# Kernel optimization log

Measured on AMD Instinct MI355X. Metric: run time of the kernel, lower is better.

Reference implementation:

```python
import jax, jax.numpy as jnp
import numpy as np

B, T, H, C = 32, 2048, 200, 256

def conv1d(x, w):
    # x: [B, T, Cin], w: [K, Cin, Cout], padding SAME, stride 1
    return jax.lax.conv_general_dilated(x, w, (1,), 'SAME',
                                        dimension_numbers=('NWC', 'WIO', 'NWC'))

def reverse_sequence(x, lengths):
    # tf.reverse_sequence along time axis 1
    t = jnp.arange(x.shape[1])[None, :]          # [1, T]
    L = lengths[:, None]                          # [B, 1]
    idx = jnp.where(t < L, L - 1 - t, t)          # [B, T]
    return jnp.take_along_axis(x, idx[:, :, None], axis=1)

def lstm(x, lengths, W, b):
    # BasicLSTMCell: gates [i, j, f, o], forget_bias=1.0
    xT = jnp.transpose(x, (1, 0, 2))              # [T, B, C]
    c0 = jnp.zeros((x.shape[0], H), x.dtype)
    h0 = jnp.zeros((x.shape[0], H), x.dtype)
    def step(carry, inp):
        c, h = carry
        xt, t = inp
        z = jnp.concatenate([xt, h], -1) @ W + b  # [B, 4H]
        i, j, f, o = jnp.split(z, 4, axis=-1)
        c_new = c * jax.nn.sigmoid(f + 1.0) + jax.nn.sigmoid(i) * jnp.tanh(j)
        h_new = jnp.tanh(c_new) * jax.nn.sigmoid(o)
        m = (t < lengths)[:, None]
        c2 = jnp.where(m, c_new, c)
        h2 = jnp.where(m, h_new, h)
        out = jnp.where(m, h_new, jnp.zeros_like(h_new))
        return (c2, h2), out
    _, ys = jax.lax.scan(step, (c0, h0), (xT, jnp.arange(xT.shape[0])))
    return jnp.transpose(ys, (1, 0, 2))           # [B, T, H]

def setup_inputs() -> dict:
    key = jax.random.key(0)
    ks = jax.random.split(key, 12)
    s = lambda k, shape, fan_in: jax.random.normal(k, shape, jnp.float32) * (1.0 / np.sqrt(fan_in))
    return {
        'signals': jax.random.normal(ks[0], (B, T, 1), jnp.float32),
        'sig_length': jax.random.randint(ks[1], (B,), T // 2, T + 1),
        'k1w': s(ks[2], (1, 1, C), 1),
        'k1aw': s(ks[3], (1, 1, C), 1),
        'k1ab': jnp.zeros((C,), jnp.float32),
        'k2w': s(ks[4], (3, C, C), 3 * C),
        'k3w': s(ks[5], (1, C, C), C),
        'Wf': s(ks[6], (C + H, 4 * H), C + H),
        'bf': jnp.zeros((4 * H,), jnp.float32),
        'Wb': s(ks[7], (C + H, 4 * H), C + H),
        'bb': jnp.zeros((4 * H,), jnp.float32),
        'Wd': s(ks[8], (2 * H, 5), 2 * H),
        'bd': jnp.zeros((5,), jnp.float32),
    }

def reference(signals, sig_length, k1w, k1aw, k1ab, k2w, k3w, Wf, bf, Wb, bb, Wd, bd):
    # resBlock
    conv1 = jax.nn.relu(conv1d(signals, k1w))
    conv1a = jax.nn.relu(conv1d(signals, k1aw) + k1ab)
    conv2 = jax.nn.relu(conv1d(conv1, k2w))
    conv3 = jax.nn.relu(conv1d(conv2, k3w))
    enc = conv3 + conv1a                               # [B, T, 256]
    # bidirectional LSTM
    fw = lstm(enc, sig_length, Wf, bf)                 # [B, T, 200]
    x_rev = reverse_sequence(enc, sig_length)
    bw = reverse_sequence(lstm(x_rev, sig_length, Wb, bb), sig_length)
    bi = jnp.concatenate([fw, bw], -1)                 # [B, T, 400]
    # dense decode to 5 logits (4 bases + blank)
    logits = bi @ Wd + bd                              # [B, T, 5]
    return logits
```

## Files before the change

### kernel.cpp

```cpp
#include <hip/hip_runtime.h>
#include <cstdint>

#define T_LEN 2048
#define NB    32
#define NROWS (NB*T_LEN)
#define HH    200
#define G4    800
#define TB    128
#define SB    8
#define XWSZ  ((size_t)64 * TB * 800)

typedef _Float16 f16;
typedef _Float16 f16x2 __attribute__((ext_vector_type(2)));
typedef _Float16 f16x8 __attribute__((ext_vector_type(8)));
typedef float   floatx4 __attribute__((ext_vector_type(4)));

#define GLD_LDS16(g, l) __builtin_amdgcn_global_load_lds( \
    (const __attribute__((address_space(1))) void*)(g), \
    (__attribute__((address_space(3))) void*)(l), 16, 0, 0)

static __device__ __forceinline__ unsigned short f2h(float x) {
  f16 h = (f16)x; return __builtin_bit_cast(unsigned short, h);
}
static __device__ __forceinline__ float dot2f(unsigned int a, unsigned int b, float c) {
  return __builtin_amdgcn_fdot2(__builtin_bit_cast(f16x2, a),
                                __builtin_bit_cast(f16x2, b), c, false);
}
static __device__ __forceinline__ float sigm(float x) {
  return __builtin_amdgcn_rcpf(1.f + __expf(-x));
}
static __device__ __forceinline__ float tanh_fast(float x) {
  return 1.f - 2.f * __builtin_amdgcn_rcpf(__expf(2.f * x) + 1.f);
}

__global__ void pq_kernel(const float* __restrict__ k1w, const float* __restrict__ k2w,
                          float* __restrict__ PQ) {
  int id = blockIdx.x * 256 + threadIdx.x;
  int pq = id / 768;
  int rem = id % 768;
  int wdt = rem / 256;
  int co  = rem % 256;
  float acc = 0.f;
  for (int ci = 0; ci < 256; ++ci) {
    float k = k1w[ci];
    float kk = pq ? fmaxf(-k, 0.f) : fmaxf(k, 0.f);
    acc += kk * k2w[((size_t)wdt * 256 + ci) * 256 + co];
  }
  PQ[id] = acc;
}

__global__ void prep_kernel(const float* __restrict__ k3w,
                            const float* __restrict__ Wf, const float* __restrict__ bfv,
                            const float* __restrict__ Wb, const float* __restrict__ bbv,
                            unsigned short* __restrict__ K3h, unsigned short* __restrict__ Wx2,
                            unsigned short* __restrict__ WhK, float* __restrict__ bcat) {
  int id = blockIdx.x * 256 + threadIdx.x;
  if (id < 65536) {
    K3h[id] = f2h(k3w[(id & 255) * 256 + (id >> 8)]);
    return;
  }
  id -= 65536;
  if (id < 409600) {
    int dirv = id / 204800;
    int r = id % 204800;
    int c = r >> 8, k = r & 255;
    int n = c >> 2, q = c & 3;
    int g = q * 200 + n;
    const float* W = dirv ? Wb : Wf;
    Wx2[id] = f2h(W[k * 800 + g]);
    return;
  }
  id -= 409600;
  if (id < 320000) {
    int rec = id / 160;
    int m   = id % 160;
    int g   = m / 40, j = m % 40;
    int n   = rec % 200;
    int t2  = rec / 200;
    int s   = t2 % 5, dirv = t2 / 5;
    int k   = s * 40 + j;
    const float* W = dirv ? Wb : Wf;
    WhK[id] = f2h(W[(256 + k) * 800 + (g * 200 + n)]);
    return;
  }
  id -= 320000;
  if (id < 1600) {
    int dirv = id / 800;
    int c = id % 800;
    int n = c >> 2, q = c & 3;
    int g = q * 200 + n;
    bcat[id] = (dirv ? bbv : bfv)[g] + (q == 2 ? 1.f : 0.f);
  }
}

__global__ void conv2_kernel(const float* __restrict__ s, const float* __restrict__ PQ,
                             unsigned short* __restrict__ C2) {
  int row = blockIdx.x;
  int co  = threadIdx.x;
  int t = row & (T_LEN - 1);
  float s0 = s[row];
  float sm = (t > 0)         ? s[row - 1] : 0.f;
  float sp = (t < T_LEN - 1) ? s[row + 1] : 0.f;
  const float* P = PQ;
  const float* Q = PQ + 768;
  float acc = 0.f;
  float a, m;
  a = fmaxf(sm, 0.f); m = fmaxf(-sm, 0.f);
  acc += a * P[0*256+co] + m * Q[0*256+co];
  a = fmaxf(s0, 0.f); m = fmaxf(-s0, 0.f);
  acc += a * P[1*256+co] + m * Q[1*256+co];
  a = fmaxf(sp, 0.f); m = fmaxf(-sp, 0.f);
  acc += a * P[2*256+co] + m * Q[2*256+co];
  C2[(size_t)row * 256 + co] = f2h(fmaxf(acc, 0.f));
}

__global__ __launch_bounds__(256, 2) void gemm_kernel(
    const unsigned short* __restrict__ Ag, const unsigned short* __restrict__ Bg0,
    int N, int ntiles, int mode,
    unsigned short* __restrict__ Outp,
    const float* __restrict__ bias, const float* __restrict__ Sg,
    const float* __restrict__ k1aw, const float* __restrict__ k1ab,
    const int* __restrict__ lens, int t0)
{
  __shared__ __align__(16) unsigned short Bl[128*128];
  __shared__ __align__(16) unsigned short Al[128*40];
  __shared__ int rowsrc[128];
  int tid = threadIdx.x;
  int tm = blockIdx.x / ntiles, tn = blockIdx.x % ntiles;
  int col0 = tn * 128;
  int lane = tid & 63, wv = tid >> 6;
  int quad = lane >> 4, l16 = lane & 15;
  int wrow = (wv & 1) * 64, wcol = (wv >> 1) * 64;

  int dirv = 0;
  if (mode == 2) dirv = tm >> 5;
  const unsigned short* Bg = Bg0 + (size_t)dirv * 204800;

  if (tid < 128) {
    int r;
    if (mode == 2) {
      int m = tm * 128 + tid;
      int ch = m >> 7;
      int ls = m & 127;
      int b = ch & 31, dd = ch >> 5;
      int L = lens[b]; L = (L < 0) ? 0 : ((L > T_LEN) ? T_LEN : L);
      int t = t0 + ls;
      int src = dd ? (L - 1 - t) : t;
      src = (src < 0) ? 0 : ((src > T_LEN - 1) ? (T_LEN - 1) : src);
      r = b * T_LEN + src;
    } else {
      r = tm * 128 + tid;
    }
    rowsrc[tid] = r;
  }

  floatx4 acc[16];
  #pragma unroll
  for (int i = 0; i < 16; ++i) acc[i] = (floatx4){0.f,0.f,0.f,0.f};

  for (int ph = 0; ph < 2; ++ph) {
    __syncthreads();
    #pragma unroll
    for (int it = 0; it < 8; ++it) {
      int idx = it * 256 + tid;
      int n  = idx >> 4;
      int k8 = idx & 15;
      int nn = col0 + n;
      uint4 v = (uint4){0u,0u,0u,0u};
      if (nn < N) v = *(const uint4*)(Bg + (size_t)nn * 256 + ph * 128 + k8 * 8);
      *(uint4*)(&Bl[n * 128 + ((k8 ^ (n & 7)) * 8)]) = v;
    }
    for (int kb2 = 0; kb2 < 4; ++kb2) {
      int kb = ph * 4 + kb2;
      __syncthreads();
      #pragma unroll
      for (int i = 0; i < 2; ++i) {
        int c2 = i * 256 + tid;
        int r = c2 >> 2, kc = (c2 & 3) * 8;
        uint4 v = *(const uint4*)(Ag + (size_t)rowsrc[r] * 256 + kb * 32 + kc);
        *(uint4*)(&Al[r * 40 + kc]) = v;
      }
      __syncthreads();
      f16x8 af[4], bfr[4];
      #pragma unroll
      for (int mt = 0; mt < 4; ++mt)
        af[mt] = *(const f16x8*)(&Al[(wrow + mt*16 + l16) * 40 + quad * 8]);
      #pragma unroll
      for (int nt = 0; nt < 4; ++nt) {
        int nl = wcol + nt*16 + l16;
        int c = kb2 * 4 + quad;
        bfr[nt] = *(const f16x8*)(&Bl[nl * 128 + ((c ^ (nl & 7)) * 8)]);
      }
      #pragma unroll
      for (int mt = 0; mt < 4; ++mt)
        #pragma unroll
        for (int nt = 0; nt < 4; ++nt)
          acc[mt*4+nt] = __builtin_amdgcn_mfma_f32_16x16x32_f16(af[mt], bfr[nt], acc[mt*4+nt], 0, 0, 0);
    }
  }
  #pragma unroll
  for (int mt = 0; mt < 4; ++mt) {
    #pragma unroll
    for (int nt = 0; nt < 4; ++nt) {
      floatx4 v = acc[mt*4+nt];
      int col = col0 + wcol + nt*16 + l16;
      if (col < N) {
        #pragma unroll
        for (int r = 0; r < 4; ++r) {
          int row = tm * 128 + wrow + mt*16 + quad*4 + r;
          float x = v[r];
          float o;
          if (mode == 0) {
            float sv = Sg[row];
            float a1 = sv * k1aw[col] + k1ab[col];
            o = fmaxf(x, 0.f) + fmaxf(a1, 0.f);
          } else {
            o = x + bias[dirv * 800 + col];
          }
          Outp[(size_t)row * N + col] = f2h(o);
        }
      }
    }
  }
}

__global__ __launch_bounds__(1024, 4)
void mega_kernel(
    const unsigned short* __restrict__ Eg,
    const unsigned short* __restrict__ Wx2,
    unsigned short* __restrict__ XWbuf,
    const float* __restrict__ bcat,
    const unsigned short* __restrict__ WhK,
    const int* __restrict__ lens,
    unsigned short* __restrict__ fwH, unsigned short* __restrict__ bwH,
    float* __restrict__ cState, unsigned short* __restrict__ hState,
    int k)
{
  __shared__ __align__(16) unsigned short xw_lds[2][SB*800];
  __shared__ __align__(16) unsigned short hist[SB*200];
  __shared__ __align__(16) unsigned short himg[2][200];
  __shared__ __align__(16) floatx4 zp[800];
  __shared__ __align__(16) unsigned short Bl[128*128];
  __shared__ __align__(16) unsigned short Al[128*40];
  __shared__ int rowsrc[128];

  int tid = threadIdx.x;
  int t0 = k * TB;

  if (blockIdx.x < 64) {
    int ch  = blockIdx.x;
    int dir = ch >> 5;
    int b   = ch & 31;
    int L = lens[b];
    L = (L < 0) ? 0 : ((L > T_LEN) ? T_LEN : L);
    int tend = t0 + TB; if (tend > L) tend = L;
    bool worker = tid < 1000;
    int s = tid / 200;
    int n = tid - s * 200;

    if (tid < 200) ((unsigned int*)himg)[tid] = 0u;

    float c = 0.f;
    unsigned short last_h = 0;
    if (tid < 200 && t0 > 0) {
      c = cState[ch * HH + tid];
      last_h = hState[ch * HH + tid];
    }
    __syncthreads();
    if (tid < 200 && t0 > 0) himg[0][tid] = last_h;

    unsigned int w[80];
    if (worker) {
      const uint4* wp = (const uint4*)(WhK + ((size_t)((dir * 5 + s) * 200 + n)) * 160);
      #pragma unroll
      for (int r = 0; r < 20; ++r) {
        uint4 v = wp[r];
        w[4*r+0] = v.x; w[4*r+1] = v.y; w[4*r+2] = v.z; w[4*r+3] = v.w;
      }
      #pragma unroll
      for (int r = 0; r < 80; ++r)
        asm volatile("" : "+v"(w[r]));
    }

    unsigned short* Hd = dir ? bwH : fwH;
    const unsigned short* XWc = XWbuf + (size_t)(k & 1) * XWSZ + ((size_t)ch * TB) * 800;

    if (t0 < tend && tid < 800)
      GLD_LDS16(XWc + (size_t)tid * 8, &xw_lds[0][tid * 8]);
    __syncthreads();

    int buf = 0, cur = 0;
    int prev_tb = -1, prev_cnt = 0;

    for (int tb = t0; tb < tend; tb += SB) {
      int cnt = tend - tb; if (cnt > SB) cnt = SB;
      for (int sl = 0; sl < cnt; ++sl) {
        if (sl == 0) {
          int ntb = tb + SB;
          if ((ntb - t0) < TB && tid < 800) {
            const unsigned short* src = XWc + (size_t)(ntb - t0) * 800;
            GLD_LDS16(src + (size_t)tid * 8, &xw_lds[buf ^ 1][tid * 8]);
          }
          if (prev_tb >= 0) {
            int pcnt = prev_cnt;
            if (tid < pcnt * 25) {
              int srow = dir ? (pcnt - 1 - tid / 25) : (tid / 25);
              uint4 v = *(const uint4*)&hist[srow*200 + (tid % 25)*8];
              size_t base = dir ? ((size_t)(b*T_LEN + (L - prev_tb - pcnt)))*HH
                                : ((size_t)(b*T_LEN + prev_tb))*HH;
              *(uint4*)(Hd + base + (size_t)tid*8) = v;
            }
          }
        }
        float a0 = 0.f, a1 = 0.f, a2 = 0.f, a3 = 0.f;
        if (worker) {
          const uint4* hp = (const uint4*)(&himg[cur][s * 40]);
          #pragma unroll
          for (int r = 0; r < 5; ++r) {
            uint4 hv = hp[r];
            int d = r * 4;
            a0 = dot2f(hv.x, w[d],      a0); a1 = dot2f(hv.x, w[20 + d], a1);
            a2 = dot2f(hv.x, w[40 + d], a2); a3 = dot2f(hv.x, w[60 + d], a3);
            a0 = dot2f(hv.y, w[d + 1],  a0); a1 = dot2f(hv.y, w[21 + d], a1);
            a2 = dot2f(hv.y, w[41 + d], a2); a3 = dot2f(hv.y, w[61 + d], a3);
            a0 = dot2f(hv.z, w[d + 2],  a0); a1 = dot2f(hv.z, w[22 + d], a1);
            a2 = dot2f(hv.z, w[42 + d], a2); a3 = dot2f(hv.z, w[62 + d], a3);
            a0 = dot2f(hv.w, w[d + 3],  a0); a1 = dot2f(hv.w, w[23 + d], a1);
            a2 = dot2f(hv.w, w[43 + d], a2); a3 = dot2f(hv.w, w[63 + d], a3);
          }
          if (s != 0) {
            floatx4 z; z[0] = a0; z[1] = a1; z[2] = a2; z[3] = a3;
            zp[(s - 1) * 200 + n] = z;
          }
        }
        __syncthreads();
        if (tid < 200) {
          floatx4 p0 = zp[tid], p1 = zp[200 + tid], p2 = zp[400 + tid], p3 = zp[600 + tid];
          uint2 xv = *(const uint2*)&xw_lds[buf][sl*800 + 4*tid];
          f16x2 xa = __builtin_bit_cast(f16x2, xv.x);
          f16x2 xb = __builtin_bit_cast(f16x2, xv.y);
          float zi = a0 + p0[0] + p1[0] + p2[0] + p3[0] + (float)xa[0];
          float zj = a1 + p0[1] + p1[1] + p2[1] + p3[1] + (float)xa[1];
          float zf = a2 + p0[2] + p1[2] + p2[2] + p3[2] + (float)xb[0];
          float zo = a3 + p0[3] + p1[3] + p2[3] + p3[3] + (float)xb[1];
          c = c * sigm(zf) + sigm(zi) * tanh_fast(zj);
          float h = tanh_fast(c) * sigm(zo);
          unsigned short hh = f2h(h);
          last_h = hh;
          himg[cur ^ 1][tid] = hh;
          hist[sl*200 + tid] = hh;
        }
        cur ^= 1;
        __syncthreads();
      }
      prev_tb = tb; prev_cnt = cnt; buf ^= 1;
    }
    if (prev_tb >= 0) {
      int pcnt = prev_cnt;
      if (tid < pcnt * 25) {
        int srow = dir ? (pcnt - 1 - tid / 25) : (tid / 25);
        uint4 v = *(const uint4*)&hist[srow*200 + (tid % 25)*8];
        size_t base = dir ? ((size_t)(b*T_LEN + (L - prev_tb - pcnt)))*HH
                          : ((size_t)(b*T_LEN + prev_tb))*HH;
        *(uint4*)(Hd + base + (size_t)tid*8) = v;
      }
    }
    if (tid < 200) {
      cState[ch * HH + tid] = c;
      hState[ch * HH + tid] = last_h;
    }
    return;
  }

  int tgem = t0 + TB;
  if (tgem >= T_LEN) return;
  unsigned short* Outp = XWbuf + (size_t)((k + 1) & 1) * XWSZ;
  int lane = tid & 63, wv = tid >> 6;
  int quad = lane >> 4, l16 = lane & 15;
  int wrow = (wv & 1) * 64, wcol = (wv >> 1) * 64;

  for (int task = blockIdx.x - 64; task < 448; task += 150) {
    int tm = task / 7, tn = task % 7;
    int col0 = tn * 128;
    int dirv = tm >> 5;
    const unsigned short* Bg = Wx2 + (size_t)dirv * 204800;

    __syncthreads();
    if (tid < 128) {
      int m = tm * 128 + tid;
      int chn = m >> 7;
      int ls = m & 127;
      int bb = chn & 31, dd = chn >> 5;
      int L = lens[bb]; L = (L < 0) ? 0 : ((L > T_LEN) ? T_LEN : L);
      int t = tgem + ls;
      int src = dd ? (L - 1 - t) : t;
      src = (src < 0) ? 0 : ((src > T_LEN - 1) ? (T_LEN - 1) : src);
      rowsrc[tid] = bb * T_LEN + src;
    }

    floatx4 acc[16];
    #pragma unroll
    for (int i = 0; i < 16; ++i) acc[i] = (floatx4){0.f,0.f,0.f,0.f};

    for (int ph = 0; ph < 2; ++ph) {
      __syncthreads();
      if (tid < 256) {
        #pragma unroll
        for (int it = 0; it < 8; ++it) {
          int idx = it * 256 + tid;
          int nl = idx >> 4;
          int k8 = idx & 15;
          int nn = col0 + nl;
          uint4 v = (uint4){0u,0u,0u,0u};
          if (nn < 800) v = *(const uint4*)(Bg + (size_t)nn * 256 + ph * 128 + k8 * 8);
          *(uint4*)(&Bl[nl * 128 + ((k8 ^ (nl & 7)) * 8)]) = v;
        }
      }
      for (int kb2 = 0; kb2 < 4; ++kb2) {
        int kb = ph * 4 + kb2;
        __syncthreads();
        if (tid < 256) {
          #pragma unroll
          for (int i = 0; i < 2; ++i) {
            int c2 = i * 256 + tid;
            int r = c2 >> 2, kc = (c2 & 3) * 8;
            uint4 v = *(const uint4*)(Eg + (size_t)rowsrc[r] * 256 + kb * 32 + kc);
            *(uint4*)(&Al[r * 40 + kc]) = v;
          }
        }
        __syncthreads();
        if (tid < 256) {
          f16x8 af[4], bfr[4];
          #pragma unroll
          for (int mt = 0; mt < 4; ++mt)
            af[mt] = *(const f16x8*)(&Al[(wrow + mt*16 + l16) * 40 + quad * 8]);
          #pragma unroll
          for (int nt = 0; nt < 4; ++nt) {
            int nl = wcol + nt*16 + l16;
            int cx = kb2 * 4 + quad;
            bfr[nt] = *(const f16x8*)(&Bl[nl * 128 + ((cx ^ (nl & 7)) * 8)]);
          }
          #pragma unroll
          for (int mt = 0; mt < 4; ++mt)
            #pragma unroll
            for (int nt = 0; nt < 4; ++nt)
              acc[mt*4+nt] = __builtin_amdgcn_mfma_f32_16x16x32_f16(af[mt], bfr[nt], acc[mt*4+nt], 0, 0, 0);
        }
      }
    }
    if (tid < 256) {
      #pragma unroll
      for (int mt = 0; mt < 4; ++mt) {
        #pragma unroll
        for (int nt = 0; nt < 4; ++nt) {
          floatx4 v = acc[mt*4+nt];
          int col = col0 + wcol + nt*16 + l16;
          if (col < 800) {
            #pragma unroll
            for (int r = 0; r < 4; ++r) {
              int row = tm * 128 + wrow + mt*16 + quad*4 + r;
              Outp[(size_t)row * 800 + col] = f2h(v[r] + bcat[dirv * 800 + col]);
            }
          }
        }
      }
    }
  }
}

__global__ __launch_bounds__(256) void out_kernel(
    const unsigned short* __restrict__ fwH, const unsigned short* __restrict__ bwH,
    const float* __restrict__ Wd, const float* __restrict__ bd, float* __restrict__ out)
{
  __shared__ float wd[2000];
  int tid = threadIdx.x;
  for (int i = tid; i < 2000; i += 256) wd[i] = Wd[i];
  __syncthreads();
  int row = blockIdx.x * 256 + tid;
  float acc0 = bd[0], acc1 = bd[1], acc2 = bd[2], acc3 = bd[3], acc4 = bd[4];
  const unsigned int* fu = (const unsigned int*)(fwH + (size_t)row * HH);
  const unsigned int* bu = (const unsigned int*)(bwH + (size_t)row * HH);
  #pragma unroll 4
  for (int i = 0; i < 100; ++i) {
    f16x2 pf = __builtin_bit_cast(f16x2, fu[i]);
    f16x2 pb = __builtin_bit_cast(f16x2, bu[i]);
    int k = 2 * i;
    float f0 = (float)pf[0], f1 = (float)pf[1];
    float b0 = (float)pb[0], b1 = (float)pb[1];
    const float* w0 = &wd[k*5];
    const float* w1 = &wd[(k+1)*5];
    const float* w2 = &wd[(200+k)*5];
    const float* w3 = &wd[(201+k)*5];
    acc0 += f0*w0[0] + f1*w1[0] + b0*w2[0] + b1*w3[0];
    acc1 += f0*w0[1] + f1*w1[1] + b0*w2[1] + b1*w3[1];
    acc2 += f0*w0[2] + f1*w1[2] + b0*w2[2] + b1*w3[2];
    acc3 += f0*w0[3] + f1*w1[3] + b0*w2[3] + b1*w3[3];
    acc4 += f0*w0[4] + f1*w1[4] + b0*w2[4] + b1*w3[4];
  }
  float* o = out + (size_t)row * 5;
  o[0]=acc0; o[1]=acc1; o[2]=acc2; o[3]=acc3; o[4]=acc4;
}

extern "C" void kernel_launch(void* const* d_in, const int* in_sizes, int n_in,
                              void* d_out, int out_size, void* d_ws, size_t ws_size,
                              hipStream_t stream)
{
  const float* signals = (const float*)d_in[0];
  const int*   lens    = (const int*)  d_in[1];
  const float* k1w     = (const float*)d_in[2];
  const float* k1aw    = (const float*)d_in[3];
  const float* k1ab    = (const float*)d_in[4];
  const float* k2w     = (const float*)d_in[5];
  const float* k3w     = (const float*)d_in[6];
  const float* Wf      = (const float*)d_in[7];
  const float* bf      = (const float*)d_in[8];
  const float* Wb      = (const float*)d_in[9];
  const float* bb      = (const float*)d_in[10];
  const float* Wd      = (const float*)d_in[11];
  const float* bd      = (const float*)d_in[12];
  float* out = (float*)d_out;
  char* ws = (char*)d_ws;

  size_t szC2   = (size_t)NROWS * 256 * 2;
  size_t szXWb  = 2 * XWSZ * 2;
  size_t szA    = (szC2 > szXWb) ? szC2 : szXWb;
  size_t oA   = 0;
  size_t oE   = oA   + szA;
  size_t oFw  = oE   + (size_t)NROWS*256*2;
  size_t oBw  = oFw  + (size_t)NROWS*HH*2;
  size_t oWhK = oBw  + (size_t)NROWS*HH*2;
  size_t oWx2 = oWhK + (size_t)320000*2;
  size_t oK3  = oWx2 + (size_t)2*256*800*2;
  size_t oPQ  = oK3  + (size_t)256*256*2;
  size_t oBc  = oPQ  + 1536*4;
  size_t oCst = oBc  + 1600*4;
  size_t oHst = oCst + (size_t)64*HH*4;
  size_t total= oHst + (size_t)64*HH*2;
  if (ws_size < total) return;

  unsigned short* C2    = (unsigned short*)(ws + oA);
  unsigned short* XWbuf = (unsigned short*)(ws + oA);
  unsigned short* E     = (unsigned short*)(ws + oE);
  unsigned short* fwH   = (unsigned short*)(ws + oFw);
  unsigned short* bwH   = (unsigned short*)(ws + oBw);
  unsigned short* WhK   = (unsigned short*)(ws + oWhK);
  unsigned short* Wx2   = (unsigned short*)(ws + oWx2);
  unsigned short* K3h   = (unsigned short*)(ws + oK3);
  float* PQ     = (float*)(ws + oPQ);
  float* bcat   = (float*)(ws + oBc);
  float* cState = (float*)(ws + oCst);
  unsigned short* hState = (unsigned short*)(ws + oHst);

  (void)hipMemsetAsync(fwH, 0, (size_t)2*NROWS*HH*2, stream);
  pq_kernel  <<<6,     256, 0, stream>>>(k1w, k2w, PQ);
  prep_kernel<<<3113,  256, 0, stream>>>(k3w, Wf, bf, Wb, bb, K3h, Wx2, WhK, bcat);
  conv2_kernel<<<NROWS, 256, 0, stream>>>(signals, PQ, C2);
  gemm_kernel<<<1024,  256, 0, stream>>>(C2, K3h, 256, 2, 0, E, nullptr, signals, k1aw, k1ab, nullptr, 0);
  gemm_kernel<<<448,   256, 0, stream>>>(E, Wx2, 800, 7, 2, XWbuf, bcat, nullptr, nullptr, nullptr, lens, 0);
  for (int k = 0; k < T_LEN / TB; ++k) {
    mega_kernel<<<214, 1024, 0, stream>>>(E, Wx2, XWbuf, bcat, WhK, lens, fwH, bwH, cState, hState, k);
  }
  out_kernel <<<256,   256, 0, stream>>>(fwH, bwH, Wd, bd, out);
}
```

Baseline: 2.347 ms.

## Process two time chunks per mega_kernel launch using a four-buffer XW ring

Each mega_kernel launch now runs the recurrence across nc consecutive 128-step chunks and has the GEMM blocks precompute input projections for the next nc chunks. XW buffering grows to four slots when the workspace allows it. This halves the number of launches and grid-wide sync points, cutting per-launch overhead and the cost of reloading weights into registers. In exchange it needs more workspace and the GEMM work per launch is larger, which could unbalance the recurrent and GEMM blocks.

```diff
diff --git a/kernel.cpp b/kernel.cpp
--- a/kernel.cpp
+++ b/kernel.cpp
@@ -234,7 +234,7 @@
     const int* __restrict__ lens,
     unsigned short* __restrict__ fwH, unsigned short* __restrict__ bwH,
     float* __restrict__ cState, unsigned short* __restrict__ hState,
-    int k)
+    int k, int nc, int bmask)
 {
   __shared__ __align__(16) unsigned short xw_lds[2][SB*800];
   __shared__ __align__(16) unsigned short hist[SB*200];
@@ -245,7 +245,6 @@
   __shared__ int rowsrc[128];
 
   int tid = threadIdx.x;
-  int t0 = k * TB;
 
   if (blockIdx.x < 64) {
     int ch  = blockIdx.x;
@@ -253,10 +252,10 @@
     int b   = ch & 31;
     int L = lens[b];
     L = (L < 0) ? 0 : ((L > T_LEN) ? T_LEN : L);
-    int tend = t0 + TB; if (tend > L) tend = L;
     bool worker = tid < 1000;
     int s = tid / 200;
     int n = tid - s * 200;
+    int t0 = k * TB;
 
     if (tid < 200) ((unsigned int*)himg)[tid] = 0u;
 
@@ -283,77 +282,82 @@
     }
 
     unsigned short* Hd = dir ? bwH : fwH;
-    const unsigned short* XWc = XWbuf + (size_t)(k & 1) * XWSZ + ((size_t)ch * TB) * 800;
-
-    if (t0 < tend && tid < 800)
-      GLD_LDS16(XWc + (size_t)tid * 8, &xw_lds[0][tid * 8]);
-    __syncthreads();
-
-    int buf = 0, cur = 0;
+    int cur = 0;
     int prev_tb = -1, prev_cnt = 0;
 
-    for (int tb = t0; tb < tend; tb += SB) {
-      int cnt = tend - tb; if (cnt > SB) cnt = SB;
-      for (int sl = 0; sl < cnt; ++sl) {
-        if (sl == 0) {
-          int ntb = tb + SB;
-          if ((ntb - t0) < TB && tid < 800) {
-            const unsigned short* src = XWc + (size_t)(ntb - t0) * 800;
-            GLD_LDS16(src + (size_t)tid * 8, &xw_lds[buf ^ 1][tid * 8]);
-          }
-          if (prev_tb >= 0) {
-            int pcnt = prev_cnt;
-            if (tid < pcnt * 25) {
-              int srow = dir ? (pcnt - 1 - tid / 25) : (tid / 25);
-              uint4 v = *(const uint4*)&hist[srow*200 + (tid % 25)*8];
-              size_t base = dir ? ((size_t)(b*T_LEN + (L - prev_tb - pcnt)))*HH
-                                : ((size_t)(b*T_LEN + prev_tb))*HH;
-              *(uint4*)(Hd + base + (size_t)tid*8) = v;
+    for (int kk = k; kk < k + nc; ++kk) {
+      int t0c = kk * TB;
+      int tend = t0c + TB; if (tend > L) tend = L;
+      const unsigned short* XWc = XWbuf + (size_t)(kk & bmask) * XWSZ + ((size_t)ch * TB) * 800;
+
+      if (t0c < tend && tid < 800)
+        GLD_LDS16(XWc + (size_t)tid * 8, &xw_lds[0][tid * 8]);
+      __syncthreads();
+
+      int buf = 0;
+      for (int tb = t0c; tb < tend; tb += SB) {
+        int cnt = tend - tb; if (cnt > SB) cnt = SB;
+        for (int sl = 0; sl < cnt; ++sl) {
+          if (sl == 0) {
+            int ntb = tb + SB;
+            if ((ntb - t0c) < TB && tid < 800) {
+              const unsigned short* src = XWc + (size_t)(ntb - t0c) * 800;
+              GLD_LDS16(src + (size_t)tid * 8, &xw_lds[buf ^ 1][tid * 8]);
             }
-          }
+            if (prev_tb >= 0) {
+              int pcnt = prev_cnt;
+              if (tid < pcnt * 25) {
+                int srow = dir ? (pcnt - 1 - tid / 25) : (tid / 25);
+                uint4 v = *(const uint4*)&hist[srow*200 + (tid % 25)*8];
+                size_t base = dir ? ((size_t)(b*T_LEN + (L - prev_tb - pcnt)))*HH
+                                  : ((size_t)(b*T_LEN + prev_tb))*HH;
+                *(uint4*)(Hd + base + (size_t)tid*8) = v;
+              }
+            }
+          }
+          float a0 = 0.f, a1 = 0.f, a2 = 0.f, a3 = 0.f;
+          if (worker) {
+            const uint4* hp = (const uint4*)(&himg[cur][s * 40]);
+            #pragma unroll
+            for (int r = 0; r < 5; ++r) {
+              uint4 hv = hp[r];
+              int d = r * 4;
+              a0 = dot2f(hv.x, w[d],      a0); a1 = dot2f(hv.x, w[20 + d], a1);
+              a2 = dot2f(hv.x, w[40 + d], a2); a3 = dot2f(hv.x, w[60 + d], a3);
+              a0 = dot2f(hv.y, w[d + 1],  a0); a1 = dot2f(hv.y, w[21 + d], a1);
+              a2 = dot2f(hv.y, w[41 + d], a2); a3 = dot2f(hv.y, w[61 + d], a3);
+              a0 = dot2f(hv.z, w[d + 2],  a0); a1 = dot2f(hv.z, w[22 + d], a1);
+              a2 = dot2f(hv.z, w[42 + d], a2); a3 = dot2f(hv.z, w[62 + d], a3);
+              a0 = dot2f(hv.w, w[d + 3],  a0); a1 = dot2f(hv.w, w[23 + d], a1);
+              a2 = dot2f(hv.w, w[43 + d], a2); a3 = dot2f(hv.w, w[63 + d], a3);
+            }
+            if (s != 0) {
+              floatx4 z; z[0] = a0; z[1] = a1; z[2] = a2; z[3] = a3;
+              zp[(s - 1) * 200 + n] = z;
+            }
+          }
+          __syncthreads();
+          if (tid < 200) {
+            floatx4 p0 = zp[tid], p1 = zp[200 + tid], p2 = zp[400 + tid], p3 = zp[600 + tid];
+            uint2 xv = *(const uint2*)&xw_lds[buf][sl*800 + 4*tid];
+            f16x2 xa = __builtin_bit_cast(f16x2, xv.x);
+            f16x2 xb = __builtin_bit_cast(f16x2, xv.y);
+            float zi = a0 + p0[0] + p1[0] + p2[0] + p3[0] + (float)xa[0];
+            float zj = a1 + p0[1] + p1[1] + p2[1] + p3[1] + (float)xa[1];
+            float zf = a2 + p0[2] + p1[2] + p2[2] + p3[2] + (float)xb[0];
+            float zo = a3 + p0[3] + p1[3] + p2[3] + p3[3] + (float)xb[1];
+            c = c * sigm(zf) + sigm(zi) * tanh_fast(zj);
+            float h = tanh_fast(c) * sigm(zo);
+            unsigned short hh = f2h(h);
+            last_h = hh;
+            himg[cur ^ 1][tid] = hh;
+            hist[sl*200 + tid] = hh;
+          }
+          cur ^= 1;
+          __syncthreads();
         }
-        float a0 = 0.f, a1 = 0.f, a2 = 0.f, a3 = 0.f;
-        if (worker) {
-          const uint4* hp = (const uint4*)(&himg[cur][s * 40]);
-          #pragma unroll
-          for (int r = 0; r < 5; ++r) {
-            uint4 hv = hp[r];
-            int d = r * 4;
-            a0 = dot2f(hv.x, w[d],      a0); a1 = dot2f(hv.x, w[20 + d], a1);
-            a2 = dot2f(hv.x, w[40 + d], a2); a3 = dot2f(hv.x, w[60 + d], a3);
-            a0 = dot2f(hv.y, w[d + 1],  a0); a1 = dot2f(hv.y, w[21 + d], a1);
-            a2 = dot2f(hv.y, w[41 + d], a2); a3 = dot2f(hv.y, w[61 + d], a3);
-            a0 = dot2f(hv.z, w[d + 2],  a0); a1 = dot2f(hv.z, w[22 + d], a1);
-            a2 = dot2f(hv.z, w[42 + d], a2); a3 = dot2f(hv.z, w[62 + d], a3);
-            a0 = dot2f(hv.w, w[d + 3],  a0); a1 = dot2f(hv.w, w[23 + d], a1);
-            a2 = dot2f(hv.w, w[43 + d], a2); a3 = dot2f(hv.w, w[63 + d], a3);
-          }
-          if (s != 0) {
-            floatx4 z; z[0] = a0; z[1] = a1; z[2] = a2; z[3] = a3;
-            zp[(s - 1) * 200 + n] = z;
-          }
-        }
-        __syncthreads();
-        if (tid < 200) {
-          floatx4 p0 = zp[tid], p1 = zp[200 + tid], p2 = zp[400 + tid], p3 = zp[600 + tid];
-          uint2 xv = *(const uint2*)&xw_lds[buf][sl*800 + 4*tid];
-          f16x2 xa = __builtin_bit_cast(f16x2, xv.x);
-          f16x2 xb = __builtin_bit_cast(f16x2, xv.y);
-          float zi = a0 + p0[0] + p1[0] + p2[0] + p3[0] + (float)xa[0];
-          float zj = a1 + p0[1] + p1[1] + p2[1] + p3[1] + (float)xa[1];
-          float zf = a2 + p0[2] + p1[2] + p2[2] + p3[2] + (float)xb[0];
-          float zo = a3 + p0[3] + p1[3] + p2[3] + p3[3] + (float)xb[1];
-          c = c * sigm(zf) + sigm(zi) * tanh_fast(zj);
-          float h = tanh_fast(c) * sigm(zo);
-          unsigned short hh = f2h(h);
-          last_h = hh;
-          himg[cur ^ 1][tid] = hh;
-          hist[sl*200 + tid] = hh;
-        }
-        cur ^= 1;
-        __syncthreads();
-      }
-      prev_tb = tb; prev_cnt = cnt; buf ^= 1;
+        prev_tb = tb; prev_cnt = cnt; buf ^= 1;
+      }
     }
     if (prev_tb >= 0) {
       int pcnt = prev_cnt;
@@ -372,15 +376,18 @@
     return;
   }
 
-  int tgem = t0 + TB;
-  if (tgem >= T_LEN) return;
-  unsigned short* Outp = XWbuf + (size_t)((k + 1) & 1) * XWSZ;
   int lane = tid & 63, wv = tid >> 6;
   int quad = lane >> 4, l16 = lane & 15;
   int wrow = (wv & 1) * 64, wcol = (wv >> 1) * 64;
 
-  for (int task = blockIdx.x - 64; task < 448; task += 150) {
-    int tm = task / 7, tn = task % 7;
+  for (int task = blockIdx.x - 64; task < 448 * nc; task += 150) {
+    int ct  = task / 448;
+    int rem = task - ct * 448;
+    int kk  = k + nc + ct;
+    int tgem = kk * TB;
+    if (tgem >= T_LEN) break;
+    unsigned short* Outp = XWbuf + (size_t)(kk & bmask) * XWSZ;
+    int tm = rem / 7, tn = rem % 7;
     int col0 = tn * 128;
     int dirv = tm >> 5;
     const unsigned short* Bg = Wx2 + (size_t)dirv * 204800;
@@ -521,22 +528,31 @@
   float* out = (float*)d_out;
   char* ws = (char*)d_ws;
 
-  size_t szC2   = (size_t)NROWS * 256 * 2;
-  size_t szXWb  = 2 * XWSZ * 2;
-  size_t szA    = (szC2 > szXWb) ? szC2 : szXWb;
-  size_t oA   = 0;
-  size_t oE   = oA   + szA;
-  size_t oFw  = oE   + (size_t)NROWS*256*2;
-  size_t oBw  = oFw  + (size_t)NROWS*HH*2;
-  size_t oWhK = oBw  + (size_t)NROWS*HH*2;
-  size_t oWx2 = oWhK + (size_t)320000*2;
-  size_t oK3  = oWx2 + (size_t)2*256*800*2;
-  size_t oPQ  = oK3  + (size_t)256*256*2;
-  size_t oBc  = oPQ  + 1536*4;
-  size_t oCst = oBc  + 1600*4;
-  size_t oHst = oCst + (size_t)64*HH*4;
-  size_t total= oHst + (size_t)64*HH*2;
-  if (ws_size < total) return;
+  size_t szC2 = (size_t)NROWS * 256 * 2;
+  size_t XWbytes = XWSZ * 2;
+
+  int nbuf = 4;
+  size_t oA, oE, oFw, oBw, oWhK, oWx2, oK3, oPQ, oBc, oCst, oHst, total;
+  for (;;) {
+    size_t szXWb = (size_t)nbuf * XWbytes;
+    size_t szA   = (szC2 > szXWb) ? szC2 : szXWb;
+    oA   = 0;
+    oE   = oA   + szA;
+    oFw  = oE   + (size_t)NROWS*256*2;
+    oBw  = oFw  + (size_t)NROWS*HH*2;
+    oWhK = oBw  + (size_t)NROWS*HH*2;
+    oWx2 = oWhK + (size_t)320000*2;
+    oK3  = oWx2 + (size_t)2*256*800*2;
+    oPQ  = oK3  + (size_t)256*256*2;
+    oBc  = oPQ  + 1536*4;
+    oCst = oBc  + 1600*4;
+    oHst = oCst + (size_t)64*HH*4;
+    total= oHst + (size_t)64*HH*2;
+    if (ws_size >= total) break;
+    if (nbuf == 2) return;
+    nbuf = 2;
+  }
+  int nc = nbuf / 2, bmask = nbuf - 1;
 
   unsigned short* C2    = (unsigned short*)(ws + oA);
   unsigned short* XWbuf = (unsigned short*)(ws + oA);
@@ -556,9 +572,12 @@
   prep_kernel<<<3113,  256, 0, stream>>>(k3w, Wf, bf, Wb, bb, K3h, Wx2, WhK, bcat);
   conv2_kernel<<<NROWS, 256, 0, stream>>>(signals, PQ, C2);
   gemm_kernel<<<1024,  256, 0, stream>>>(C2, K3h, 256, 2, 0, E, nullptr, signals, k1aw, k1ab, nullptr, 0);
-  gemm_kernel<<<448,   256, 0, stream>>>(E, Wx2, 800, 7, 2, XWbuf, bcat, nullptr, nullptr, nullptr, lens, 0);
-  for (int k = 0; k < T_LEN / TB; ++k) {
-    mega_kernel<<<214, 1024, 0, stream>>>(E, Wx2, XWbuf, bcat, WhK, lens, fwH, bwH, cState, hState, k);
+  for (int j = 0; j < nc; ++j)
+    gemm_kernel<<<448, 256, 0, stream>>>(E, Wx2, 800, 7, 2, XWbuf + (size_t)j * XWSZ,
+                                         bcat, nullptr, nullptr, nullptr, lens, j * TB);
+  for (int k = 0; k < T_LEN / TB; k += nc) {
+    mega_kernel<<<214, 1024, 0, stream>>>(E, Wx2, XWbuf, bcat, WhK, lens,
+                                          fwH, bwH, cState, hState, k, nc, bmask);
   }
   out_kernel <<<256,   256, 0, stream>>>(fwH, bwH, Wd, bd, out);
 }
```

After: 2.279 ms. 2.9% less time.
